# Performance work log

Hardware: AMD Instinct MI355X
Metric: run time of the kernel (lower is better)

The kernel has to match this reference:

```python
import jax, jax.numpy as jnp
import numpy as np

BN_EPS = 1e-5


def _conv1x1(x, w, b):
    # x: (B,C,H,W), w: (O,C) -> (B,O,H,W)
    return jnp.einsum('bchw,oc->bohw', x, w) + b[None, :, None, None]


def _maxpool2x2(x):
    b, c, h, w = x.shape
    return x.reshape(b, c, h // 2, 2, w // 2, 2).max(axis=(3, 5))


def _minmax(a, axis):
    mn = a.min(axis=axis, keepdims=True)
    mx = a.max(axis=axis, keepdims=True)
    return (a - mn) / (mx - mn)


def _gaussian_bias(row, dh, dw):
    # Vectorized version of the original per-row numpy double loop.
    sigma = max(1, int(min(dh, dw) / 10))
    j = jnp.arange(row)
    cx = ((j // 4) // dw).astype(jnp.float32)   # floor(j/4/down_col)
    cy = ((j // 4) % dw).astype(jnp.float32)    # floor(j/4) % down_col
    mx = jnp.arange(dh, dtype=jnp.float32)[None, :, None]
    my = jnp.arange(dw, dtype=jnp.float32)[None, None, :]
    d2 = (mx - cx[:, None, None]) ** 2 + (my - cy[:, None, None]) ** 2
    return (-d2 / (2.0 * sigma * sigma)).reshape(row, dh * dw)  # (row, col)


def reference(x, g_w, g_b, theta_w, theta_b, phi_w, phi_b, w_w, w_b,
              bn_gamma, bn_beta, bn_mean, bn_var):
    b, c, H, W = x.shape
    ic = g_w.shape[0]
    dh, dw = H // 2, W // 2
    row, col = H * W, dh * dw

    g_x = _maxpool2x2(_conv1x1(x, g_w, g_b)).reshape(b, ic, col).transpose(0, 2, 1)  # (b,col,ic)
    theta = _conv1x1(x, theta_w, theta_b).reshape(b, ic, row).transpose(0, 2, 1)     # (b,row,ic)
    phi = _maxpool2x2(_conv1x1(x, phi_w, phi_b)).reshape(b, ic, col)                 # (b,ic,col)

    f = jnp.einsum('bri,bic->brc', theta, phi)  # (b,row,col)
    temp = _gaussian_bias(row, dh, dw)[None]    # (1,row,col), same for all batch

    f = (_minmax(f, -1) - 1.0) + (_minmax(temp, -1) - 1.0)
    f_div_C = jax.nn.softmax(f, axis=-1)

    g_x = _minmax(g_x, 1)  # min/max over positions
    y = jnp.einsum('brc,bci->bri', f_div_C, g_x)        # (b,row,ic)
    y = y.transpose(0, 2, 1).reshape(b, ic, H, W)

    W_y = _conv1x1(y, w_w, w_b)
    W_y = bn_gamma[None, :, None, None] * (W_y - bn_mean[None, :, None, None]) \
        * jax.lax.rsqrt(bn_var + BN_EPS)[None, :, None, None] + bn_beta[None, :, None, None]
    return W_y + x


def setup_inputs() -> dict:
    key = jax.random.key(0)
    ks = jax.random.split(key, 13)
    B, C, IC, H, W = 8, 64, 32, 64, 64
    s = 0.1
    return {
        'x': jax.random.normal(ks[0], (B, C, H, W), jnp.float32),
        'g_w': jax.random.normal(ks[1], (IC, C), jnp.float32) * s,
        'g_b': jax.random.normal(ks[2], (IC,), jnp.float32) * s,
        'theta_w': jax.random.normal(ks[3], (IC, C), jnp.float32) * s,
        'theta_b': jax.random.normal(ks[4], (IC,), jnp.float32) * s,
        'phi_w': jax.random.normal(ks[5], (IC, C), jnp.float32) * s,
        'phi_b': jax.random.normal(ks[6], (IC,), jnp.float32) * s,
        'w_w': jax.random.normal(ks[7], (C, IC), jnp.float32) * s,
        'w_b': jax.random.normal(ks[8], (C,), jnp.float32) * s,
        'bn_gamma': jax.random.uniform(ks[9], (C,), jnp.float32, 0.5, 1.5),
        'bn_beta': jax.random.normal(ks[10], (C,), jnp.float32) * s,
        'bn_mean': jax.random.normal(ks[11], (C,), jnp.float32) * s,
        'bn_var': jax.random.uniform(ks[12], (C,), jnp.float32, 0.5, 1.5),
    }
```

## Files before the change

kernel.cpp:

```cpp
#include <hip/hip_runtime.h>
#include <math.h>

#define RFL(x) __builtin_amdgcn_readfirstlane(x)

static constexpr int Bn = 8, Cn = 64, ICn = 32, Hn = 64, Wn = 64;
static constexpr int ROW = Hn * Wn;
static constexpr int COLn = 1024;

static constexpr size_t OFF_THETA = 0;
static constexpr size_t OFF_PHI   = (size_t)Bn * ROW * ICn;
static constexpr size_t OFF_G     = OFF_PHI + (size_t)Bn * ICn * COLn;
static constexpr size_t OFF_Y     = OFF_G + (size_t)Bn * COLn * ICn;
static constexpr size_t OFF_GMN   = OFF_Y + (size_t)Bn * ROW * ICn;
static constexpr size_t OFF_GINV  = OFF_GMN + (size_t)Bn * ICn;

__device__ __forceinline__ void gload_lds16(const float* src, float* ldsbase) {
    __builtin_amdgcn_global_load_lds(
        (const __attribute__((address_space(1))) unsigned int*)(const void*)src,
        (__attribute__((address_space(3))) unsigned int*)(void*)ldsbase, 16, 0, 0);
}

__global__ __launch_bounds__(256) void k_conv3(
    const float* __restrict__ x,
    const float* __restrict__ wth, const float* __restrict__ bth,
    const float* __restrict__ wph, const float* __restrict__ bph,
    const float* __restrict__ wg,  const float* __restrict__ bg,
    float* __restrict__ theta, float* __restrict__ phi, float* __restrict__ g)
{
    const int tid  = threadIdx.x;
    const int lane = tid & 63;
    const int ty   = RFL(tid >> 6);
    const int b    = blockIdx.z;
    const int pc   = blockIdx.x * 64 + lane;
    const int phh  = pc >> 5, pww = pc & 31;
    const int o0   = blockIdx.y * 8 + ty * 2;

    const float* xb = x + (size_t)b * Cn * ROW;
    const int pos0 = (2 * phh) * Wn + 2 * pww;

    float accT[2][4], accP[2][4], accG[2][4];
    #pragma unroll
    for (int j = 0; j < 2; ++j)
        #pragma unroll
        for (int q = 0; q < 4; ++q) { accT[j][q] = 0.f; accP[j][q] = 0.f; accG[j][q] = 0.f; }

    float2 pf0[8], pf1[8];
    #pragma unroll
    for (int i = 0; i < 8; ++i) {
        const float* xc = xb + (size_t)i * ROW + pos0;
        pf0[i] = *(const float2*)xc;
        pf1[i] = *(const float2*)(xc + Wn);
    }
    #pragma unroll 1
    for (int cb = 0; cb < Cn; cb += 8) {
        float2 c0[8], c1[8];
        #pragma unroll
        for (int i = 0; i < 8; ++i) { c0[i] = pf0[i]; c1[i] = pf1[i]; }
        if (cb + 8 < Cn) {
            #pragma unroll
            for (int i = 0; i < 8; ++i) {
                const float* xc = xb + (size_t)(cb + 8 + i) * ROW + pos0;
                pf0[i] = *(const float2*)xc;
                pf1[i] = *(const float2*)(xc + Wn);
            }
        }
        #pragma unroll
        for (int i = 0; i < 8; ++i) {
            const int c = cb + i;
            const float xv0 = c0[i].x, xv1 = c0[i].y, xv2 = c1[i].x, xv3 = c1[i].y;
            #pragma unroll
            for (int j = 0; j < 2; ++j) {
                const int o = o0 + j;
                const float wt  = wth[o * Cn + c];
                const float wp  = wph[o * Cn + c];
                const float wgv = wg [o * Cn + c];
                accT[j][0] = fmaf(wt, xv0, accT[j][0]); accT[j][1] = fmaf(wt, xv1, accT[j][1]);
                accT[j][2] = fmaf(wt, xv2, accT[j][2]); accT[j][3] = fmaf(wt, xv3, accT[j][3]);
                accP[j][0] = fmaf(wp, xv0, accP[j][0]); accP[j][1] = fmaf(wp, xv1, accP[j][1]);
                accP[j][2] = fmaf(wp, xv2, accP[j][2]); accP[j][3] = fmaf(wp, xv3, accP[j][3]);
                accG[j][0] = fmaf(wgv, xv0, accG[j][0]); accG[j][1] = fmaf(wgv, xv1, accG[j][1]);
                accG[j][2] = fmaf(wgv, xv2, accG[j][2]); accG[j][3] = fmaf(wgv, xv3, accG[j][3]);
            }
        }
    }

    const int prow[4] = {pos0, pos0 + 1, pos0 + Wn, pos0 + Wn + 1};
    const float bt0 = bth[o0], bt1 = bth[o0 + 1];
    #pragma unroll
    for (int q = 0; q < 4; ++q) {
        float2 tv;
        tv.x = accT[0][q] + bt0; tv.y = accT[1][q] + bt1;
        *(float2*)&theta[((size_t)b * ROW + prow[q]) * ICn + o0] = tv;
    }
    float2 gv;
    #pragma unroll
    for (int j = 0; j < 2; ++j) {
        const int o = o0 + j;
        float mp = fmaxf(fmaxf(accP[j][0], accP[j][1]), fmaxf(accP[j][2], accP[j][3]));
        phi[((size_t)b * ICn + o) * COLn + pc] = mp + bph[o];
        float mg = fmaxf(fmaxf(accG[j][0], accG[j][1]), fmaxf(accG[j][2], accG[j][3]));
        (&gv.x)[j] = mg + bg[o];
    }
    *(float2*)&g[((size_t)b * COLn + pc) * ICn + o0] = gv;
}

__global__ __launch_bounds__(256) void k_gminmax(
    const float* __restrict__ g, float* __restrict__ gmn, float* __restrict__ ginv)
{
    __shared__ float red[2][4][4];
    const int tid = threadIdx.x;
    const int icq = blockIdx.x & 7, b = blockIdx.x >> 3;
    float4 mn4 = make_float4(3.4e38f, 3.4e38f, 3.4e38f, 3.4e38f);
    float4 mx4 = make_float4(-3.4e38f, -3.4e38f, -3.4e38f, -3.4e38f);
    #pragma unroll
    for (int i = 0; i < 4; ++i) {
        float4 v = *(const float4*)&g[((size_t)b * COLn + i * 256 + tid) * ICn + icq * 4];
        mn4.x = fminf(mn4.x, v.x); mn4.y = fminf(mn4.y, v.y);
        mn4.z = fminf(mn4.z, v.z); mn4.w = fminf(mn4.w, v.w);
        mx4.x = fmaxf(mx4.x, v.x); mx4.y = fmaxf(mx4.y, v.y);
        mx4.z = fmaxf(mx4.z, v.z); mx4.w = fmaxf(mx4.w, v.w);
    }
    #pragma unroll
    for (int m = 1; m < 64; m <<= 1) {
        mn4.x = fminf(mn4.x, __shfl_xor(mn4.x, m)); mx4.x = fmaxf(mx4.x, __shfl_xor(mx4.x, m));
        mn4.y = fminf(mn4.y, __shfl_xor(mn4.y, m)); mx4.y = fmaxf(mx4.y, __shfl_xor(mx4.y, m));
        mn4.z = fminf(mn4.z, __shfl_xor(mn4.z, m)); mx4.z = fmaxf(mx4.z, __shfl_xor(mx4.z, m));
        mn4.w = fminf(mn4.w, __shfl_xor(mn4.w, m)); mx4.w = fmaxf(mx4.w, __shfl_xor(mx4.w, m));
    }
    const int wv = tid >> 6;
    if ((tid & 63) == 0) {
        red[0][wv][0] = mn4.x; red[0][wv][1] = mn4.y; red[0][wv][2] = mn4.z; red[0][wv][3] = mn4.w;
        red[1][wv][0] = mx4.x; red[1][wv][1] = mx4.y; red[1][wv][2] = mx4.z; red[1][wv][3] = mx4.w;
    }
    __syncthreads();
    if (tid < 4) {
        float mn = fminf(fminf(red[0][0][tid], red[0][1][tid]),
                         fminf(red[0][2][tid], red[0][3][tid]));
        float mx = fmaxf(fmaxf(red[1][0][tid], red[1][1][tid]),
                         fmaxf(red[1][2][tid], red[1][3][tid]));
        gmn[b * ICn + icq * 4 + tid] = mn;
        ginv[b * ICn + icq * 4 + tid] = 1.0f / (mx - mn);
    }
}

#define RPW 8
#define CCH 256
#define PCOL(c) ((c) ^ ((((c) >> 5) & 7) << 2))

__global__ __launch_bounds__(256, 2) void k_attn(
    const float* __restrict__ theta, const float* __restrict__ phi,
    const float* __restrict__ g, const float* __restrict__ gmn,
    const float* __restrict__ ginv, float* __restrict__ y)
{
    __shared__ float phiS[32 * CCH];
    __shared__ float pS[4][RPW][CCH];

    const int tid  = threadIdx.x;
    const int lane = tid & 63;
    const int wid  = RFL(tid >> 6);
    const int b    = blockIdx.y;
    const int icq  = lane & 7;
    const int csplit = lane >> 3;
    const int colbase = lane * 4;

    const float* phiB = phi + (size_t)b * ICn * COLn;
    const float* gB   = g + (size_t)b * COLn * ICn;
    const float4 gmn4 = *(const float4*)(gmn + b * ICn + icq * 4);
    const float4 giv4 = *(const float4*)(ginv + b * ICn + icq * 4);

    const int row0 = blockIdx.x * 32 + wid * RPW;
    const float* thB = theta + ((size_t)b * ROW + row0) * ICn;
    float* const pSw = &pS[wid][0][0];

    float4 f4[RPW][4];
    #pragma unroll
    for (int r = 0; r < RPW; ++r) {
        f4[r][0] = make_float4(0.f, 0.f, 0.f, 0.f);
        f4[r][1] = make_float4(0.f, 0.f, 0.f, 0.f);
        f4[r][2] = make_float4(0.f, 0.f, 0.f, 0.f);
        f4[r][3] = make_float4(0.f, 0.f, 0.f, 0.f);
    }

    #define PHASEA_CH(CH) { \
        __syncthreads(); \
        _Pragma("unroll") \
        for (int i = 0; i < 8; ++i) { \
            const int k = wid * 8 + i; \
            gload_lds16(phiB + (size_t)k * COLn + (CH) * CCH + lane * 4, &phiS[k * CCH]); \
        } \
        __syncthreads(); \
        _Pragma("unroll 8") \
        for (int k = 0; k < 32; ++k) { \
            float4 pv = *(const float4*)&phiS[k * CCH + colbase]; \
            _Pragma("unroll") \
            for (int r = 0; r < RPW; ++r) { \
                const float t = thB[r * ICn + k]; \
                f4[r][CH].x = fmaf(t, pv.x, f4[r][CH].x); \
                f4[r][CH].y = fmaf(t, pv.y, f4[r][CH].y); \
                f4[r][CH].z = fmaf(t, pv.z, f4[r][CH].z); \
                f4[r][CH].w = fmaf(t, pv.w, f4[r][CH].w); \
            } \
        } }
    PHASEA_CH(0) PHASEA_CH(1) PHASEA_CH(2) PHASEA_CH(3)
    #undef PHASEA_CH

    float rinv[RPW];
    #pragma unroll
    for (int r = 0; r < RPW; ++r) {
        const int row = row0 + r;
        float mn = 3.4e38f, mx = -3.4e38f;
        #pragma unroll
        for (int ch = 0; ch < 4; ++ch) {
            float4 v = f4[r][ch];
            mn = fminf(mn, fminf(fminf(v.x, v.y), fminf(v.z, v.w)));
            mx = fmaxf(mx, fmaxf(fmaxf(v.x, v.y), fmaxf(v.z, v.w)));
        }
        #pragma unroll
        for (int m = 1; m < 64; m <<= 1) {
            mn = fminf(mn, __shfl_xor(mn, m));
            mx = fmaxf(mx, __shfl_xor(mx, m));
        }
        const float finv = 1.0f / (mx - mn);
        const float cx = (float)(row >> 7);
        const float cy = (float)((row >> 2) & 31);
        const float mdx = fmaxf(cx * cx, (31.0f - cx) * (31.0f - cx));
        const float mdy = fmaxf(cy * cy, (31.0f - cy) * (31.0f - cy));
        const float dinv = 1.0f / (mdx + mdy);
        const float c0 = -1.0f - mn * finv;

        float dx2[4], dy2[4];
        #pragma unroll
        for (int u = 0; u < 4; ++u) {
            const float dx = (float)(u * 8 + csplit) - cx;
            dx2[u] = dx * dx;
            const float dy = (float)(icq * 4 + u) - cy;
            dy2[u] = dy * dy;
        }
        float s0 = 0.f, s1 = 0.f;
        #pragma unroll
        for (int ch = 0; ch < 4; ++ch) {
            float4 v = f4[r][ch];
            v.x = __expf(fmaf(v.x, finv, fmaf(dx2[ch] + dy2[0], -dinv, c0)));
            v.y = __expf(fmaf(v.y, finv, fmaf(dx2[ch] + dy2[1], -dinv, c0)));
            v.z = __expf(fmaf(v.z, finv, fmaf(dx2[ch] + dy2[2], -dinv, c0)));
            v.w = __expf(fmaf(v.w, finv, fmaf(dx2[ch] + dy2[3], -dinv, c0)));
            f4[r][ch] = v;
            s0 += v.x + v.y; s1 += v.z + v.w;
        }
        float s = s0 + s1;
        #pragma unroll
        for (int m = 1; m < 64; m <<= 1) s += __shfl_xor(s, m);
        rinv[r] = 1.0f / s;
    }

    float4 y4[RPW];
    #pragma unroll
    for (int r = 0; r < RPW; ++r) y4[r] = make_float4(0.f, 0.f, 0.f, 0.f);

    #define PHASEC_CH(CH) { \
        _Pragma("unroll") \
        for (int r = 0; r < RPW; ++r) \
            *(float4*)&pSw[r * CCH + PCOL(colbase)] = f4[r][CH]; \
        asm volatile("s_waitcnt lgkmcnt(0)" ::: "memory"); \
        const float* gch = gB + (size_t)(CH) * CCH * ICn + icq * 4; \
        _Pragma("unroll 2") \
        for (int cc4 = 0; cc4 < 32; cc4 += 4) { \
            const int cl = csplit * 32 + cc4; \
            float4 pb[RPW]; \
            _Pragma("unroll") \
            for (int r = 0; r < RPW; ++r) \
                pb[r] = *(const float4*)&pSw[r * CCH + PCOL(cl)]; \
            const float* gp = gch + (size_t)cl * ICn; \
            float4 g4; \
            _Pragma("unroll") \
            for (int u = 0; u < 4; ++u) { \
                g4 = *(const float4*)(gp + u * ICn); \
                _Pragma("unroll") \
                for (int r = 0; r < RPW; ++r) { \
                    const float pv = (&pb[r].x)[u]; \
                    y4[r].x = fmaf(pv, g4.x, y4[r].x); \
                    y4[r].y = fmaf(pv, g4.y, y4[r].y); \
                    y4[r].z = fmaf(pv, g4.z, y4[r].z); \
                    y4[r].w = fmaf(pv, g4.w, y4[r].w); \
                } \
            } \
        } \
        asm volatile("" ::: "memory"); }
    PHASEC_CH(0) PHASEC_CH(1) PHASEC_CH(2) PHASEC_CH(3)
    #undef PHASEC_CH

    #pragma unroll
    for (int r = 0; r < RPW; ++r) {
        float4 v = y4[r];
        #pragma unroll
        for (int m = 8; m < 64; m <<= 1) {
            v.x += __shfl_xor(v.x, m);
            v.y += __shfl_xor(v.y, m);
            v.z += __shfl_xor(v.z, m);
            v.w += __shfl_xor(v.w, m);
        }
        if (csplit == 0) {
            const float rs = rinv[r];
            float4 o;
            o.x = v.x * rs * giv4.x - gmn4.x * giv4.x;
            o.y = v.y * rs * giv4.y - gmn4.y * giv4.y;
            o.z = v.z * rs * giv4.z - gmn4.z * giv4.z;
            o.w = v.w * rs * giv4.w - gmn4.w * giv4.w;
            *(float4*)&y[((size_t)b * ROW + row0 + r) * ICn + icq * 4] = o;
        }
    }
}

__global__ __launch_bounds__(256) void k_out(
    const float* __restrict__ y, const float* __restrict__ x,
    const float* __restrict__ ww, const float* __restrict__ wb,
    const float* __restrict__ gam, const float* __restrict__ bet,
    const float* __restrict__ mean, const float* __restrict__ var,
    float* __restrict__ out)
{
    const int tid = threadIdx.x, lane = tid & 63;
    const int ty = RFL(tid >> 6);
    const int b = blockIdx.z;
    const int p = blockIdx.x * 64 + lane;
    const int o0 = (blockIdx.y * 4 + ty) * 8;

    const float* yr = y + ((size_t)b * ROW + p) * ICn;
    float4 yv[8];
    #pragma unroll
    for (int i = 0; i < 8; ++i) yv[i] = *(const float4*)(yr + i * 4);

    #pragma unroll
    for (int oo = 0; oo < 8; ++oo) {
        const int o = o0 + oo;
        const float* wr = ww + o * ICn;
        float acc = 0.f;
        #pragma unroll
        for (int i = 0; i < 8; ++i) {
            acc = fmaf(wr[i * 4 + 0], yv[i].x, acc);
            acc = fmaf(wr[i * 4 + 1], yv[i].y, acc);
            acc = fmaf(wr[i * 4 + 2], yv[i].z, acc);
            acc = fmaf(wr[i * 4 + 3], yv[i].w, acc);
        }
        const float s = gam[o] * rsqrtf(var[o] + 1e-5f);
        const float res = s * (acc + wb[o] - mean[o]) + bet[o]
                        + x[((size_t)(b * Cn + o)) * ROW + p];
        out[((size_t)(b * Cn + o)) * ROW + p] = res;
    }
}

extern "C" void kernel_launch(void* const* d_in, const int* in_sizes, int n_in,
                              void* d_out, int out_size, void* d_ws, size_t ws_size,
                              hipStream_t stream) {
    (void)in_sizes; (void)n_in; (void)out_size; (void)ws_size;
    const float* x    = (const float*)d_in[0];
    const float* g_w  = (const float*)d_in[1];
    const float* g_b  = (const float*)d_in[2];
    const float* th_w = (const float*)d_in[3];
    const float* th_b = (const float*)d_in[4];
    const float* ph_w = (const float*)d_in[5];
    const float* ph_b = (const float*)d_in[6];
    const float* w_w  = (const float*)d_in[7];
    const float* w_b  = (const float*)d_in[8];
    const float* bng  = (const float*)d_in[9];
    const float* bnb  = (const float*)d_in[10];
    const float* bnm  = (const float*)d_in[11];
    const float* bnv  = (const float*)d_in[12];
    float* out = (float*)d_out;
    float* ws  = (float*)d_ws;

    float* theta = ws + OFF_THETA;
    float* phi   = ws + OFF_PHI;
    float* g     = ws + OFF_G;
    float* y     = ws + OFF_Y;
    float* gmn   = ws + OFF_GMN;
    float* ginv  = ws + OFF_GINV;

    hipLaunchKernelGGL(k_conv3, dim3(16, 4, 8), dim3(256), 0, stream,
                       x, th_w, th_b, ph_w, ph_b, g_w, g_b, theta, phi, g);
    hipLaunchKernelGGL(k_gminmax, dim3(64), dim3(256), 0, stream, g, gmn, ginv);
    hipLaunchKernelGGL(k_attn, dim3(128, 8), dim3(256), 0, stream,
                       theta, phi, g, gmn, ginv, y);
    hipLaunchKernelGGL(k_out, dim3(64, 2, 8), dim3(256), 0, stream,
                       y, x, w_w, w_b, bng, bnb, bnm, bnv, out);
}
```

Baseline: 176.6 us.

## Load phi directly from global in attention, one channel per thread in conv

The attention kernel no longer stages phi through LDS with async global-to-LDS loads and block barriers. Each thread now reads its four float4 phi columns straight from global memory inside the k loop, relying on L1/L2 caching and removing the 32 KB shared buffer and the syncs. Separately, the conv kernel computes one output channel per thread instead of two, using twice as many blocks. That gives more parallelism but reloads x for every channel and writes theta and g with scalar stores instead of float2 stores.

```diff
diff --git a/kernel.cpp b/kernel.cpp
--- a/kernel.cpp
+++ b/kernel.cpp
@@ -13,12 +13,6 @@
 static constexpr size_t OFF_Y     = OFF_G + (size_t)Bn * COLn * ICn;
 static constexpr size_t OFF_GMN   = OFF_Y + (size_t)Bn * ROW * ICn;
 static constexpr size_t OFF_GINV  = OFF_GMN + (size_t)Bn * ICn;
-
-__device__ __forceinline__ void gload_lds16(const float* src, float* ldsbase) {
-    __builtin_amdgcn_global_load_lds(
-        (const __attribute__((address_space(1))) unsigned int*)(const void*)src,
-        (__attribute__((address_space(3))) unsigned int*)(void*)ldsbase, 16, 0, 0);
-}
 
 __global__ __launch_bounds__(256) void k_conv3(
     const float* __restrict__ x,
@@ -33,16 +27,14 @@
     const int b    = blockIdx.z;
     const int pc   = blockIdx.x * 64 + lane;
     const int phh  = pc >> 5, pww = pc & 31;
-    const int o0   = blockIdx.y * 8 + ty * 2;
+    const int o    = blockIdx.y * 4 + ty;
 
     const float* xb = x + (size_t)b * Cn * ROW;
     const int pos0 = (2 * phh) * Wn + 2 * pww;
 
-    float accT[2][4], accP[2][4], accG[2][4];
-    #pragma unroll
-    for (int j = 0; j < 2; ++j)
-        #pragma unroll
-        for (int q = 0; q < 4; ++q) { accT[j][q] = 0.f; accP[j][q] = 0.f; accG[j][q] = 0.f; }
+    float accT[4], accP[4], accG[4];
+    #pragma unroll
+    for (int q = 0; q < 4; ++q) { accT[q] = 0.f; accP[q] = 0.f; accG[q] = 0.f; }
 
     float2 pf0[8], pf1[8];
     #pragma unroll
@@ -68,40 +60,27 @@
         for (int i = 0; i < 8; ++i) {
             const int c = cb + i;
             const float xv0 = c0[i].x, xv1 = c0[i].y, xv2 = c1[i].x, xv3 = c1[i].y;
-            #pragma unroll
-            for (int j = 0; j < 2; ++j) {
-                const int o = o0 + j;
-                const float wt  = wth[o * Cn + c];
-                const float wp  = wph[o * Cn + c];
-                const float wgv = wg [o * Cn + c];
-                accT[j][0] = fmaf(wt, xv0, accT[j][0]); accT[j][1] = fmaf(wt, xv1, accT[j][1]);
-                accT[j][2] = fmaf(wt, xv2, accT[j][2]); accT[j][3] = fmaf(wt, xv3, accT[j][3]);
-                accP[j][0] = fmaf(wp, xv0, accP[j][0]); accP[j][1] = fmaf(wp, xv1, accP[j][1]);
-                accP[j][2] = fmaf(wp, xv2, accP[j][2]); accP[j][3] = fmaf(wp, xv3, accP[j][3]);
-                accG[j][0] = fmaf(wgv, xv0, accG[j][0]); accG[j][1] = fmaf(wgv, xv1, accG[j][1]);
-                accG[j][2] = fmaf(wgv, xv2, accG[j][2]); accG[j][3] = fmaf(wgv, xv3, accG[j][3]);
-            }
+            const float wt  = wth[o * Cn + c];
+            const float wp  = wph[o * Cn + c];
+            const float wgv = wg [o * Cn + c];
+            accT[0] = fmaf(wt, xv0, accT[0]); accT[1] = fmaf(wt, xv1, accT[1]);
+            accT[2] = fmaf(wt, xv2, accT[2]); accT[3] = fmaf(wt, xv3, accT[3]);
+            accP[0] = fmaf(wp, xv0, accP[0]); accP[1] = fmaf(wp, xv1, accP[1]);
+            accP[2] = fmaf(wp, xv2, accP[2]); accP[3] = fmaf(wp, xv3, accP[3]);
+            accG[0] = fmaf(wgv, xv0, accG[0]); accG[1] = fmaf(wgv, xv1, accG[1]);
+            accG[2] = fmaf(wgv, xv2, accG[2]); accG[3] = fmaf(wgv, xv3, accG[3]);
         }
     }
 
     const int prow[4] = {pos0, pos0 + 1, pos0 + Wn, pos0 + Wn + 1};
-    const float bt0 = bth[o0], bt1 = bth[o0 + 1];
-    #pragma unroll
-    for (int q = 0; q < 4; ++q) {
-        float2 tv;
-        tv.x = accT[0][q] + bt0; tv.y = accT[1][q] + bt1;
-        *(float2*)&theta[((size_t)b * ROW + prow[q]) * ICn + o0] = tv;
-    }
-    float2 gv;
-    #pragma unroll
-    for (int j = 0; j < 2; ++j) {
-        const int o = o0 + j;
-        float mp = fmaxf(fmaxf(accP[j][0], accP[j][1]), fmaxf(accP[j][2], accP[j][3]));
-        phi[((size_t)b * ICn + o) * COLn + pc] = mp + bph[o];
-        float mg = fmaxf(fmaxf(accG[j][0], accG[j][1]), fmaxf(accG[j][2], accG[j][3]));
-        (&gv.x)[j] = mg + bg[o];
-    }
-    *(float2*)&g[((size_t)b * COLn + pc) * ICn + o0] = gv;
+    const float bt = bth[o];
+    #pragma unroll
+    for (int q = 0; q < 4; ++q)
+        theta[((size_t)b * ROW + prow[q]) * ICn + o] = accT[q] + bt;
+    float mp = fmaxf(fmaxf(accP[0], accP[1]), fmaxf(accP[2], accP[3]));
+    phi[((size_t)b * ICn + o) * COLn + pc] = mp + bph[o];
+    float mg = fmaxf(fmaxf(accG[0], accG[1]), fmaxf(accG[2], accG[3]));
+    g[((size_t)b * COLn + pc) * ICn + o] = mg + bg[o];
 }
 
 __global__ __launch_bounds__(256) void k_gminmax(
@@ -152,7 +131,6 @@
     const float* __restrict__ g, const float* __restrict__ gmn,
     const float* __restrict__ ginv, float* __restrict__ y)
 {
-    __shared__ float phiS[32 * CCH];
     __shared__ float pS[4][RPW][CCH];
 
     const int tid  = threadIdx.x;
@@ -181,28 +159,35 @@
         f4[r][3] = make_float4(0.f, 0.f, 0.f, 0.f);
     }
 
-    #define PHASEA_CH(CH) { \
-        __syncthreads(); \
-        _Pragma("unroll") \
-        for (int i = 0; i < 8; ++i) { \
-            const int k = wid * 8 + i; \
-            gload_lds16(phiB + (size_t)k * COLn + (CH) * CCH + lane * 4, &phiS[k * CCH]); \
-        } \
-        __syncthreads(); \
-        _Pragma("unroll 8") \
-        for (int k = 0; k < 32; ++k) { \
-            float4 pv = *(const float4*)&phiS[k * CCH + colbase]; \
-            _Pragma("unroll") \
-            for (int r = 0; r < RPW; ++r) { \
-                const float t = thB[r * ICn + k]; \
-                f4[r][CH].x = fmaf(t, pv.x, f4[r][CH].x); \
-                f4[r][CH].y = fmaf(t, pv.y, f4[r][CH].y); \
-                f4[r][CH].z = fmaf(t, pv.z, f4[r][CH].z); \
-                f4[r][CH].w = fmaf(t, pv.w, f4[r][CH].w); \
-            } \
-        } }
-    PHASEA_CH(0) PHASEA_CH(1) PHASEA_CH(2) PHASEA_CH(3)
-    #undef PHASEA_CH
+    const float* phiC = phiB + colbase;
+    #pragma unroll 4
+    for (int k = 0; k < 32; ++k) {
+        const float* pk = phiC + (size_t)k * COLn;
+        const float4 pv0 = *(const float4*)(pk + 0 * CCH);
+        const float4 pv1 = *(const float4*)(pk + 1 * CCH);
+        const float4 pv2 = *(const float4*)(pk + 2 * CCH);
+        const float4 pv3 = *(const float4*)(pk + 3 * CCH);
+        #pragma unroll
+        for (int r = 0; r < RPW; ++r) {
+            const float t = thB[r * ICn + k];
+            f4[r][0].x = fmaf(t, pv0.x, f4[r][0].x);
+            f4[r][0].y = fmaf(t, pv0.y, f4[r][0].y);
+            f4[r][0].z = fmaf(t, pv0.z, f4[r][0].z);
+            f4[r][0].w = fmaf(t, pv0.w, f4[r][0].w);
+            f4[r][1].x = fmaf(t, pv1.x, f4[r][1].x);
+            f4[r][1].y = fmaf(t, pv1.y, f4[r][1].y);
+            f4[r][1].z = fmaf(t, pv1.z, f4[r][1].z);
+            f4[r][1].w = fmaf(t, pv1.w, f4[r][1].w);
+            f4[r][2].x = fmaf(t, pv2.x, f4[r][2].x);
+            f4[r][2].y = fmaf(t, pv2.y, f4[r][2].y);
+            f4[r][2].z = fmaf(t, pv2.z, f4[r][2].z);
+            f4[r][2].w = fmaf(t, pv2.w, f4[r][2].w);
+            f4[r][3].x = fmaf(t, pv3.x, f4[r][3].x);
+            f4[r][3].y = fmaf(t, pv3.y, f4[r][3].y);
+            f4[r][3].z = fmaf(t, pv3.z, f4[r][3].z);
+            f4[r][3].w = fmaf(t, pv3.w, f4[r][3].w);
+        }
+    }
 
     float rinv[RPW];
     #pragma unroll
@@ -375,7 +360,7 @@
     float* gmn   = ws + OFF_GMN;
     float* ginv  = ws + OFF_GINV;
 
-    hipLaunchKernelGGL(k_conv3, dim3(16, 4, 8), dim3(256), 0, stream,
+    hipLaunchKernelGGL(k_conv3, dim3(16, 8, 8), dim3(256), 0, stream,
                        x, th_w, th_b, ph_w, ph_b, g_w, g_b, theta, phi, g);
     hipLaunchKernelGGL(k_gminmax, dim3(64), dim3(256), 0, stream, g, gmn, ginv);
     hipLaunchKernelGGL(k_attn, dim3(128, 8), dim3(256), 0, stream,
```

Result: no change. 178.6 us (+1.1%).
